# Performance work log

Hardware: AMD Instinct MI355X
Metric: run time of the kernel (lower is better)

## Reference

```python
import jax, jax.numpy as jnp
import numpy as np

VOCAB = 50000
EMBED = 256
BATCH = 16384
NUM_SAMPLED = 4096


def _log_uniform_prob(ids):
    # P(c) = (log(c+2) - log(c+1)) / log(V+1), the log-uniform sampler distribution
    ids = ids.astype(jnp.float32)
    return (jnp.log(ids + 2.0) - jnp.log(ids + 1.0)) / jnp.log(VOCAB + 1.0)


def _expected_count(ids, num_sampled):
    # unique log-uniform sampler expected count: 1 - (1 - p)^num_tries, num_tries ~= num_sampled
    p = _log_uniform_prob(ids)
    return -jnp.expm1(num_sampled * jnp.log1p(-p))


def _sigmoid_xent(logits, labels):
    # stable sigmoid cross-entropy: max(x,0) - x*z + log(1 + exp(-|x|))
    return jnp.maximum(logits, 0.0) - logits * labels + jnp.log1p(jnp.exp(-jnp.abs(logits)))


def setup_inputs() -> dict:
    key = jax.random.key(0)
    k1, k2, k3, k4 = jax.random.split(key, 4)
    embedding = jax.random.normal(k1, (BATCH, EMBED), dtype=jnp.float32)
    target_words = jax.random.randint(k2, (BATCH, 1), 0, VOCAB, dtype=jnp.int64 if jax.config.jax_enable_x64 else jnp.int32)
    sampled_ids = jax.random.randint(k3, (NUM_SAMPLED,), 0, VOCAB, dtype=jnp.int64 if jax.config.jax_enable_x64 else jnp.int32)
    # truncated-normal init with stddev 1/sqrt(embed_size), matching TruncatedNormal
    nce_weight = (jax.random.truncated_normal(k4, -2.0, 2.0, (VOCAB, EMBED), dtype=jnp.float32)
                  * (1.0 / EMBED ** 0.5))
    nce_bias = jnp.zeros((VOCAB,), dtype=jnp.float32)
    return {"embedding": embedding, "target_words": target_words,
            "sampled_ids": sampled_ids, "nce_weight": nce_weight, "nce_bias": nce_bias}


def reference(embedding, target_words, sampled_ids, nce_weight, nce_bias):
    num_sampled = sampled_ids.shape[0]
    labels = target_words[:, 0]                       # [B]

    # gather true-class rows and compute true logits (subtract_log_q=True in tf.nn.nce_loss)
    w_true = nce_weight[labels]                       # [B, D]
    true_logits = (jnp.sum(embedding * w_true, axis=-1) + nce_bias[labels]
                   - jnp.log(_expected_count(labels, num_sampled)))          # [B]

    # gather sampled rows and compute sampled logits
    w_samp = nce_weight[sampled_ids]                  # [S, D]
    sampled_logits = (jnp.einsum('bd,sd->bs', embedding, w_samp) + nce_bias[sampled_ids]
                      - jnp.log(_expected_count(sampled_ids, num_sampled)))  # [B, S]

    # sigmoid cross-entropy: true label 1, sampled labels 0; sum per example, mean over batch
    per_example = _sigmoid_xent(true_logits, 1.0) + jnp.sum(_sigmoid_xent(sampled_logits, 0.0), axis=-1)
    return jnp.mean(per_example)
```

## Files before the change

kernel.cpp:

```cpp
#include <hip/hip_runtime.h>
#include <cstdint>
#include <cstddef>

#define VOCAB 50000
#define EMBED 256
#define BATCH 16384
#define NSAMP 4096

typedef float f32x4 __attribute__((ext_vector_type(4)));
typedef int   i32x4 __attribute__((ext_vector_type(4)));
typedef int   i32x8 __attribute__((ext_vector_type(8)));


__device__ __forceinline__ f32x4 vsplat(float a) {
    f32x4 r = {a, a, a, a};
    return r;
}

__device__ __forceinline__ float log_expected_count(int id) {
    float u = 1.0f / ((float)id + 1.0f);
    float a = __logf(1.0f + u);
    float p = a * 0.09242324f;
    float ser = p * (1.0f + p * (0.5f + p * (0.33333333f + p * (0.25f + p * 0.2f))));
    float q = -(float)NSAMP * ser;
    return __logf(1.0f - __expf(q));
}

__device__ __forceinline__ float softplus_f(float x) {
    float v = __expf(-fabsf(x));
    float p = fmaf(v, 0.03215845f, -0.13606275f);
    p = fmaf(v, p, 0.28947478f);
    p = fmaf(v, p, -0.49190896f);
    p = fmaf(v, p, 0.99949556f);
    return fmaxf(x, 0.0f) + v * p;
}

__device__ __forceinline__ void softplus4_acc(f32x4 x, f32x4& vsum) {
    f32x4 ax = __builtin_elementwise_abs(x);
    f32x4 v;
    v.x = __expf(-ax.x);
    v.y = __expf(-ax.y);
    v.z = __expf(-ax.z);
    v.w = __expf(-ax.w);
    f32x4 p = __builtin_elementwise_fma(v, vsplat(0.03215845f), vsplat(-0.13606275f));
    p = __builtin_elementwise_fma(v, p, vsplat(0.28947478f));
    p = __builtin_elementwise_fma(v, p, vsplat(-0.49190896f));
    p = __builtin_elementwise_fma(v, p, vsplat(0.99949556f));
    vsum += __builtin_elementwise_max(x, vsplat(0.0f));
    vsum = __builtin_elementwise_fma(v, p, vsum);
}

__device__ __forceinline__ int pk4_fp8(float a, float b, float c, float d) {
    int v = __builtin_amdgcn_cvt_pk_fp8_f32(a, b, 0, false);
    v = __builtin_amdgcn_cvt_pk_fp8_f32(c, d, v, true);
    return v;
}



__global__ __launch_bounds__(256) void k_prep(
        const float* __restrict__ E, const int* __restrict__ tgt,
        const int* __restrict__ sids, const float* __restrict__ W,
        const float* __restrict__ bias,
        unsigned char* __restrict__ EF, unsigned char* __restrict__ BF,
        float* __restrict__ badj, double* __restrict__ pTrue)
{
    const int blk = blockIdx.x, tid = threadIdx.x;
    const int wave = tid >> 6, lane = tid & 63;

    if (blk < 1024) {
        float tsum = 0.0f;
        #pragma unroll
        for (int i = 0; i < 4; ++i) {
            int b = (blk * 4 + wave) + 4096 * i;
            int label = tgt[b];
            float4 e  = ((const float4*)(E + (size_t)b * EMBED))[lane];
            float4 wv = ((const float4*)(W + (size_t)label * EMBED))[lane];
            int pk = pk4_fp8(e.x, e.y, e.z, e.w);
            *(int*)(EF + ((b >> 4) * 4096 + (lane >> 3) * 512
                          + (b & 15) * 32 + (lane & 7) * 4)) = pk;
            float d = e.x * wv.x + e.y * wv.y + e.z * wv.z + e.w * wv.w;
            #pragma unroll
            for (int off = 32; off > 0; off >>= 1) d += __shfl_down(d, off, 64);
            if (lane == 0) {
                float tl = d + bias[label] - log_expected_count(label);
                tsum += softplus_f(-tl);
            }
        }
        __shared__ float ts[4];
        if (lane == 0) ts[wave] = tsum;
        __syncthreads();
        if (tid == 0) pTrue[blk] = (double)((ts[0] + ts[1]) + (ts[2] + ts[3]));
    } else {
        #pragma unroll
        for (int i = 0; i < 4; ++i) {
            int task = (blk - 1024) * 256 + tid + 16384 * i;
            int s = task >> 4, p = task & 15;
            int sid = sids[s];
            const float4* wr = (const float4*)(W + (size_t)sid * EMBED + p * 16);
            float4 w0 = wr[0], w1 = wr[1], w2 = wr[2], w3 = wr[3];
            int4 o;
            o.x = pk4_fp8(w0.x * 16.0f, w0.y * 16.0f, w0.z * 16.0f, w0.w * 16.0f);
            o.y = pk4_fp8(w1.x * 16.0f, w1.y * 16.0f, w1.z * 16.0f, w1.w * 16.0f);
            o.z = pk4_fp8(w2.x * 16.0f, w2.y * 16.0f, w2.z * 16.0f, w2.w * 16.0f);
            o.w = pk4_fp8(w3.x * 16.0f, w3.y * 16.0f, w3.z * 16.0f, w3.w * 16.0f);
            *(int4*)(BF + ((s >> 4) * 4096 + (p >> 1) * 512 + (p & 1) * 256
                           + (s & 15) * 16)) = o;
            if (p == 0) badj[s] = bias[sid] - log_expected_count(sid);
        }
    }
}

__global__ __launch_bounds__(512, 4) void k_gemm(
        const unsigned char* __restrict__ EF,
        const unsigned char* __restrict__ BF,
        const float* __restrict__ badj,
        double* __restrict__ pGemm)
{
    const int tid  = threadIdx.x;
    const int wave = tid >> 6;
    const int lane = tid & 63;
    const int rg   = blockIdx.x >> 4;
    const int cg   = blockIdx.x & 15;
    const int ag0  = rg * 16 + wave * 2;
    const int r16  = lane & 15;

    __shared__ unsigned char Blds[65536];
    __shared__ float wsum[8];

    i32x8 af[2][2];
    #pragma unroll
    for (int s = 0; s < 2; ++s)
        #pragma unroll
        for (int mi = 0; mi < 2; ++mi)
            af[s][mi] = *(const i32x8*)(EF + (size_t)(ag0 + mi) * 4096
                                        + s * 2048 + lane * 32);

    {
        const unsigned char* Bsrc = BF + (size_t)cg * 65536;
        #pragma unroll
        for (int it = 0; it < 8; ++it) {
            int woff = it * 8192 + wave * 1024;
            int goff = woff + lane * 16;
            __builtin_amdgcn_global_load_lds(
                (const __attribute__((address_space(1))) void*)(Bsrc + goff),
                (__attribute__((address_space(3))) void*)(Blds + woff),
                16, 0, 0);
        }
    }

    asm volatile("s_waitcnt vmcnt(0)");
    __syncthreads();

    #pragma unroll
    for (int s = 0; s < 2; ++s)
        #pragma unroll
        for (int mi = 0; mi < 2; ++mi)
            asm volatile("" : "+v"(af[s][mi]));

    f32x4 vsum = {};
    const int lbase = (lane >> 4) * 512 + r16 * 16;

    #pragma unroll 1
    for (int j = 0; j < 4; ++j) {
        float ba[4];
        #pragma unroll
        for (int ni = 0; ni < 4; ++ni)
            ba[ni] = badj[cg * 256 + j * 64 + ni * 16 + r16];

        f32x4 acc[2][4] = {};
        #pragma unroll
        for (int s = 0; s < 2; ++s) {
            i32x8 bf[4];
            #pragma unroll
            for (int ni = 0; ni < 4; ++ni) {
                const unsigned char* bp = Blds + (j * 4 + ni) * 4096
                                          + s * 2048 + lbase;
                i32x4 lo = *(const i32x4*)bp;
                i32x4 hi = *(const i32x4*)(bp + 256);
                bf[ni][0] = lo[0]; bf[ni][1] = lo[1];
                bf[ni][2] = lo[2]; bf[ni][3] = lo[3];
                bf[ni][4] = hi[0]; bf[ni][5] = hi[1];
                bf[ni][6] = hi[2]; bf[ni][7] = hi[3];
            }
            #pragma unroll
            for (int mi = 0; mi < 2; ++mi)
                #pragma unroll
                for (int ni = 0; ni < 4; ++ni)
                    acc[mi][ni] = __builtin_amdgcn_mfma_scale_f32_16x16x128_f8f6f4(
                        af[s][mi], bf[ni], acc[mi][ni],
                        0, 0,
                        0, 0x7F7F7F7F,
                        0, 0x7B7B7B7B);
        }

        #pragma unroll
        for (int mi = 0; mi < 2; ++mi)
            #pragma unroll
            for (int ni = 0; ni < 4; ++ni)
                softplus4_acc(acc[mi][ni] + ba[ni], vsum);
    }

    float lsum = (vsum.x + vsum.y) + (vsum.z + vsum.w);
    #pragma unroll
    for (int off = 32; off > 0; off >>= 1) lsum += __shfl_down(lsum, off, 64);
    if (lane == 0) wsum[wave] = lsum;
    __syncthreads();
    if (tid == 0)
        pGemm[blockIdx.x] = (double)((((wsum[0] + wsum[1]) + (wsum[2] + wsum[3]))
                                    + ((wsum[4] + wsum[5]) + (wsum[6] + wsum[7]))));
}

__global__ __launch_bounds__(256) void k_final(
        const double* __restrict__ pTrue, const double* __restrict__ pGemm,
        float* __restrict__ out)
{
    const int tid = threadIdx.x, wave = tid >> 6, lane = tid & 63;
    double s = 0.0;
    for (int i = tid; i < 1024; i += 256) s += pTrue[i];
    for (int i = tid; i < 1024; i += 256) s += pGemm[i];
    #pragma unroll
    for (int off = 32; off > 0; off >>= 1) s += __shfl_down(s, off, 64);
    __shared__ double wsum[4];
    if (lane == 0) wsum[wave] = s;
    __syncthreads();
    if (tid == 0)
        out[0] = (float)(((wsum[0] + wsum[1]) + (wsum[2] + wsum[3]))
                         * (1.0 / (double)BATCH));
}


extern "C" void kernel_launch(void* const* d_in, const int* in_sizes, int n_in,
                              void* d_out, int out_size, void* d_ws, size_t ws_size,
                              hipStream_t stream) {
    const float* emb  = (const float*)d_in[0];
    const int*   tgt  = (const int*)d_in[1];
    const int*   sids = (const int*)d_in[2];
    const float* W    = (const float*)d_in[3];
    const float* bias = (const float*)d_in[4];
    float* out = (float*)d_out;

    char* ws = (char*)d_ws;
    double*        pTrue = (double*)ws;
    double*        pGemm = (double*)(ws + 8192);
    float*         badj  = (float*)(ws + 40960);
    unsigned char* BF    = (unsigned char*)(ws + 57344);
    unsigned char* EF    = (unsigned char*)(ws + 57344 + 1048576);

    hipLaunchKernelGGL(k_prep, dim3(1088), dim3(256), 0, stream,
                       emb, tgt, sids, W, bias, EF, BF, badj, pTrue);
    hipLaunchKernelGGL(k_gemm, dim3(1024), dim3(512), 0, stream,
                       EF, BF, badj, pGemm);
    hipLaunchKernelGGL(k_final, dim3(1), dim3(256), 0, stream,
                       pTrue, pGemm, out);
}
```

Before: 129.0 us.

## Fold final reduction into GEMM via last-block atomic and reshape wave tiling

Result: slower. 141.6 us (+9.8%).

```diff
diff --git a/kernel.cpp b/kernel.cpp
--- a/kernel.cpp
+++ b/kernel.cpp
@@ -63,10 +63,13 @@
         const int* __restrict__ sids, const float* __restrict__ W,
         const float* __restrict__ bias,
         unsigned char* __restrict__ EF, unsigned char* __restrict__ BF,
-        float* __restrict__ badj, double* __restrict__ pTrue)
+        float* __restrict__ badj, double* __restrict__ pTrue,
+        unsigned int* __restrict__ cnt)
 {
     const int blk = blockIdx.x, tid = threadIdx.x;
     const int wave = tid >> 6, lane = tid & 63;
+
+    if (blk == 0 && tid == 0) *cnt = 0;
 
     if (blk < 1024) {
         float tsum = 0.0f;
@@ -115,24 +118,31 @@
         const unsigned char* __restrict__ EF,
         const unsigned char* __restrict__ BF,
         const float* __restrict__ badj,
-        double* __restrict__ pGemm)
+        const double* __restrict__ pTrue,
+        double* __restrict__ pGemm,
+        unsigned int* __restrict__ cnt,
+        float* __restrict__ out)
 {
     const int tid  = threadIdx.x;
     const int wave = tid >> 6;
     const int lane = tid & 63;
     const int rg   = blockIdx.x >> 4;
     const int cg   = blockIdx.x & 15;
-    const int ag0  = rg * 16 + wave * 2;
+    const int wr   = wave >> 1;
+    const int wc   = wave & 1;
+    const int ag0  = rg * 16 + wr * 4;
     const int r16  = lane & 15;
 
     __shared__ unsigned char Blds[65536];
-    __shared__ float wsum[8];
-
-    i32x8 af[2][2];
+    __shared__ float  wsum[8];
+    __shared__ double dsum[8];
+    __shared__ int    lastflag;
+
+    i32x8 af[2][4];
     #pragma unroll
     for (int s = 0; s < 2; ++s)
         #pragma unroll
-        for (int mi = 0; mi < 2; ++mi)
+        for (int mi = 0; mi < 4; ++mi)
             af[s][mi] = *(const i32x8*)(EF + (size_t)(ag0 + mi) * 4096
                                         + s * 2048 + lane * 32);
 
@@ -155,50 +165,39 @@
     #pragma unroll
     for (int s = 0; s < 2; ++s)
         #pragma unroll
-        for (int mi = 0; mi < 2; ++mi)
+        for (int mi = 0; mi < 4; ++mi)
             asm volatile("" : "+v"(af[s][mi]));
 
     f32x4 vsum = {};
     const int lbase = (lane >> 4) * 512 + r16 * 16;
+    const float* badj_base = badj + cg * 256 + wc * 128 + r16;
 
     #pragma unroll 1
-    for (int j = 0; j < 4; ++j) {
-        float ba[4];
-        #pragma unroll
-        for (int ni = 0; ni < 4; ++ni)
-            ba[ni] = badj[cg * 256 + j * 64 + ni * 16 + r16];
-
-        f32x4 acc[2][4] = {};
+    for (int cgi = 0; cgi < 8; ++cgi) {
+        float ba = badj_base[cgi * 16];
+
+        f32x4 acc[4] = {};
         #pragma unroll
         for (int s = 0; s < 2; ++s) {
-            i32x8 bf[4];
+            const unsigned char* bp = Blds + (wc * 8 + cgi) * 4096
+                                      + s * 2048 + lbase;
+            i32x4 lo = *(const i32x4*)bp;
+            i32x4 hi = *(const i32x4*)(bp + 256);
+            i32x8 bf;
+            bf[0] = lo[0]; bf[1] = lo[1]; bf[2] = lo[2]; bf[3] = lo[3];
+            bf[4] = hi[0]; bf[5] = hi[1]; bf[6] = hi[2]; bf[7] = hi[3];
             #pragma unroll
-            for (int ni = 0; ni < 4; ++ni) {
-                const unsigned char* bp = Blds + (j * 4 + ni) * 4096
-                                          + s * 2048 + lbase;
-                i32x4 lo = *(const i32x4*)bp;
-                i32x4 hi = *(const i32x4*)(bp + 256);
-                bf[ni][0] = lo[0]; bf[ni][1] = lo[1];
-                bf[ni][2] = lo[2]; bf[ni][3] = lo[3];
-                bf[ni][4] = hi[0]; bf[ni][5] = hi[1];
-                bf[ni][6] = hi[2]; bf[ni][7] = hi[3];
-            }
-            #pragma unroll
-            for (int mi = 0; mi < 2; ++mi)
-                #pragma unroll
-                for (int ni = 0; ni < 4; ++ni)
-                    acc[mi][ni] = __builtin_amdgcn_mfma_scale_f32_16x16x128_f8f6f4(
-                        af[s][mi], bf[ni], acc[mi][ni],
-                        0, 0,
-                        0, 0x7F7F7F7F,
-                        0, 0x7B7B7B7B);
-        }
-
-        #pragma unroll
-        for (int mi = 0; mi < 2; ++mi)
-            #pragma unroll
-            for (int ni = 0; ni < 4; ++ni)
-                softplus4_acc(acc[mi][ni] + ba[ni], vsum);
+            for (int mi = 0; mi < 4; ++mi)
+                acc[mi] = __builtin_amdgcn_mfma_scale_f32_16x16x128_f8f6f4(
+                    af[s][mi], bf, acc[mi],
+                    0, 0,
+                    0, 0x7F7F7F7F,
+                    0, 0x7B7B7B7B);
+        }
+
+        #pragma unroll
+        for (int mi = 0; mi < 4; ++mi)
+            softplus4_acc(acc[mi] + vsplat(ba), vsum);
     }
 
     float lsum = (vsum.x + vsum.y) + (vsum.z + vsum.w);
@@ -206,27 +205,30 @@
     for (int off = 32; off > 0; off >>= 1) lsum += __shfl_down(lsum, off, 64);
     if (lane == 0) wsum[wave] = lsum;
     __syncthreads();
-    if (tid == 0)
+
+    if (tid == 0) {
         pGemm[blockIdx.x] = (double)((((wsum[0] + wsum[1]) + (wsum[2] + wsum[3]))
                                     + ((wsum[4] + wsum[5]) + (wsum[6] + wsum[7]))));
-}
-
-__global__ __launch_bounds__(256) void k_final(
-        const double* __restrict__ pTrue, const double* __restrict__ pGemm,
-        float* __restrict__ out)
-{
-    const int tid = threadIdx.x, wave = tid >> 6, lane = tid & 63;
-    double s = 0.0;
-    for (int i = tid; i < 1024; i += 256) s += pTrue[i];
-    for (int i = tid; i < 1024; i += 256) s += pGemm[i];
-    #pragma unroll
-    for (int off = 32; off > 0; off >>= 1) s += __shfl_down(s, off, 64);
-    __shared__ double wsum[4];
-    if (lane == 0) wsum[wave] = s;
+        __threadfence();
+        unsigned int old = atomicAdd(cnt, 1u);
+        lastflag = (old == 1023u) ? 1 : 0;
+    }
     __syncthreads();
-    if (tid == 0)
-        out[0] = (float)(((wsum[0] + wsum[1]) + (wsum[2] + wsum[3]))
-                         * (1.0 / (double)BATCH));
+
+    if (lastflag) {
+        __threadfence();
+        double s = 0.0;
+        for (int i = tid; i < 1024; i += 512) s += pTrue[i];
+        for (int i = tid; i < 1024; i += 512) s += pGemm[i];
+        #pragma unroll
+        for (int off = 32; off > 0; off >>= 1) s += __shfl_down(s, off, 64);
+        if (lane == 0) dsum[wave] = s;
+        __syncthreads();
+        if (tid == 0)
+            out[0] = (float)(((((dsum[0] + dsum[1]) + (dsum[2] + dsum[3]))
+                             + ((dsum[4] + dsum[5]) + (dsum[6] + dsum[7])))
+                             ) * (1.0 / (double)BATCH));
+    }
 }
 
 
@@ -243,14 +245,13 @@
     char* ws = (char*)d_ws;
     double*        pTrue = (double*)ws;
     double*        pGemm = (double*)(ws + 8192);
+    unsigned int*  cnt   = (unsigned int*)(ws + 16384);
     float*         badj  = (float*)(ws + 40960);
     unsigned char* BF    = (unsigned char*)(ws + 57344);
     unsigned char* EF    = (unsigned char*)(ws + 57344 + 1048576);
 
     hipLaunchKernelGGL(k_prep, dim3(1088), dim3(256), 0, stream,
-                       emb, tgt, sids, W, bias, EF, BF, badj, pTrue);
+                       emb, tgt, sids, W, bias, EF, BF, badj, pTrue, cnt);
     hipLaunchKernelGGL(k_gemm, dim3(1024), dim3(512), 0, stream,
-                       EF, BF, badj, pGemm);
-    hipLaunchKernelGGL(k_final, dim3(1), dim3(256), 0, stream,
-                       pTrue, pGemm, out);
-}
+                       EF, BF, badj, pTrue, pGemm, cnt, out);
+}
```

## Halve GEMM block column tile to double grid and occupancy

Applied to the files above, without the earlier changes.

New measurement: 157.2 us. +21.8%, slower.

```diff
diff --git a/kernel.cpp b/kernel.cpp
--- a/kernel.cpp
+++ b/kernel.cpp
@@ -111,7 +111,7 @@
     }
 }
 
-__global__ __launch_bounds__(512, 4) void k_gemm(
+__global__ __launch_bounds__(512, 8) void k_gemm(
         const unsigned char* __restrict__ EF,
         const unsigned char* __restrict__ BF,
         const float* __restrict__ badj,
@@ -120,12 +120,12 @@
     const int tid  = threadIdx.x;
     const int wave = tid >> 6;
     const int lane = tid & 63;
-    const int rg   = blockIdx.x >> 4;
-    const int cg   = blockIdx.x & 15;
+    const int rg   = blockIdx.x >> 5;
+    const int cg2  = blockIdx.x & 31;
     const int ag0  = rg * 16 + wave * 2;
     const int r16  = lane & 15;
 
-    __shared__ unsigned char Blds[65536];
+    __shared__ unsigned char Blds[32768];
     __shared__ float wsum[8];
 
     i32x8 af[2][2];
@@ -137,9 +137,9 @@
                                         + s * 2048 + lane * 32);
 
     {
-        const unsigned char* Bsrc = BF + (size_t)cg * 65536;
-        #pragma unroll
-        for (int it = 0; it < 8; ++it) {
+        const unsigned char* Bsrc = BF + (size_t)cg2 * 32768;
+        #pragma unroll
+        for (int it = 0; it < 4; ++it) {
             int woff = it * 8192 + wave * 1024;
             int goff = woff + lane * 16;
             __builtin_amdgcn_global_load_lds(
@@ -160,45 +160,33 @@
 
     f32x4 vsum = {};
     const int lbase = (lane >> 4) * 512 + r16 * 16;
+    const float* bb = badj + cg2 * 128 + r16;
 
     #pragma unroll 1
-    for (int j = 0; j < 4; ++j) {
-        float ba[4];
-        #pragma unroll
-        for (int ni = 0; ni < 4; ++ni)
-            ba[ni] = badj[cg * 256 + j * 64 + ni * 16 + r16];
-
-        f32x4 acc[2][4] = {};
+    for (int cgi = 0; cgi < 8; ++cgi) {
+        float ba = bb[cgi * 16];
+
+        f32x4 acc[2] = {};
         #pragma unroll
         for (int s = 0; s < 2; ++s) {
-            i32x8 bf[4];
-            #pragma unroll
-            for (int ni = 0; ni < 4; ++ni) {
-                const unsigned char* bp = Blds + (j * 4 + ni) * 4096
-                                          + s * 2048 + lbase;
-                i32x4 lo = *(const i32x4*)bp;
-                i32x4 hi = *(const i32x4*)(bp + 256);
-                bf[ni][0] = lo[0]; bf[ni][1] = lo[1];
-                bf[ni][2] = lo[2]; bf[ni][3] = lo[3];
-                bf[ni][4] = hi[0]; bf[ni][5] = hi[1];
-                bf[ni][6] = hi[2]; bf[ni][7] = hi[3];
-            }
+            const unsigned char* bp = Blds + cgi * 4096 + s * 2048 + lbase;
+            i32x4 lo = *(const i32x4*)bp;
+            i32x4 hi = *(const i32x4*)(bp + 256);
+            i32x8 bf;
+            bf[0] = lo[0]; bf[1] = lo[1]; bf[2] = lo[2]; bf[3] = lo[3];
+            bf[4] = hi[0]; bf[5] = hi[1]; bf[6] = hi[2]; bf[7] = hi[3];
             #pragma unroll
             for (int mi = 0; mi < 2; ++mi)
-                #pragma unroll
-                for (int ni = 0; ni < 4; ++ni)
-                    acc[mi][ni] = __builtin_amdgcn_mfma_scale_f32_16x16x128_f8f6f4(
-                        af[s][mi], bf[ni], acc[mi][ni],
-                        0, 0,
-                        0, 0x7F7F7F7F,
-                        0, 0x7B7B7B7B);
+                acc[mi] = __builtin_amdgcn_mfma_scale_f32_16x16x128_f8f6f4(
+                    af[s][mi], bf, acc[mi],
+                    0, 0,
+                    0, 0x7F7F7F7F,
+                    0, 0x7B7B7B7B);
         }
 
         #pragma unroll
         for (int mi = 0; mi < 2; ++mi)
-            #pragma unroll
-            for (int ni = 0; ni < 4; ++ni)
-                softplus4_acc(acc[mi][ni] + ba[ni], vsum);
+            softplus4_acc(acc[mi] + vsplat(ba), vsum);
     }
 
     float lsum = (vsum.x + vsum.y) + (vsum.z + vsum.w);
@@ -218,7 +206,7 @@
     const int tid = threadIdx.x, wave = tid >> 6, lane = tid & 63;
     double s = 0.0;
     for (int i = tid; i < 1024; i += 256) s += pTrue[i];
-    for (int i = tid; i < 1024; i += 256) s += pGemm[i];
+    for (int i = tid; i < 2048; i += 256) s += pGemm[i];
     #pragma unroll
     for (int off = 32; off > 0; off >>= 1) s += __shfl_down(s, off, 64);
     __shared__ double wsum[4];
@@ -249,7 +237,7 @@
 
     hipLaunchKernelGGL(k_prep, dim3(1088), dim3(256), 0, stream,
                        emb, tgt, sids, W, bias, EF, BF, badj, pTrue);
-    hipLaunchKernelGGL(k_gemm, dim3(1024), dim3(512), 0, stream,
+    hipLaunchKernelGGL(k_gemm, dim3(2048), dim3(512), 0, stream,
                        EF, BF, badj, pGemm);
     hipLaunchKernelGGL(k_final, dim3(1), dim3(256), 0, stream,
                        pTrue, pGemm, out);
```
